# Performance work log

Measured on AMD Instinct MI355X. Metric: run time of the kernel, lower is better.

The kernel has to match this reference:

```python
import jax, jax.numpy as jnp
import numpy as np

N_NODES = 40000
N_EDGES = 640000
IN_CH, HID_CH, OUT_CH = 128, 128, 64


def setup_inputs() -> dict:
    key = jax.random.key(0)
    ks = jax.random.split(key, 8)
    x = jax.random.normal(ks[0], (N_NODES, IN_CH), dtype=jnp.float32)
    edge_index = jax.random.randint(ks[1], (2, N_EDGES), 0, N_NODES, dtype=jnp.int32)
    s = 1.0 / np.sqrt(IN_CH)
    W1_rel = jax.random.normal(ks[2], (HID_CH, IN_CH), dtype=jnp.float32) * s
    W1_root = jax.random.normal(ks[3], (HID_CH, IN_CH), dtype=jnp.float32) * s
    b1 = jnp.zeros((HID_CH,), dtype=jnp.float32)
    s2 = 1.0 / np.sqrt(HID_CH)
    W2_rel = jax.random.normal(ks[4], (OUT_CH, HID_CH), dtype=jnp.float32) * s2
    W2_root = jax.random.normal(ks[5], (OUT_CH, HID_CH), dtype=jnp.float32) * s2
    b2 = jnp.zeros((OUT_CH,), dtype=jnp.float32)
    return {"x": x, "edge_index": edge_index, "W1_rel": W1_rel, "W1_root": W1_root,
            "b1": b1, "W2_rel": W2_rel, "W2_root": W2_root, "b2": b2}


def graph_conv(x, edge_index, W_rel, W_root, b):
    # PyG GraphConv (aggr='add'): out_i = W_rel @ (sum_{j->i} x_j) + W_root @ x_i + b
    src, dst = edge_index[0], edge_index[1]
    agg = jax.ops.segment_sum(x[src], dst, num_segments=x.shape[0])  # [N, d_in]
    return agg @ W_rel.T + x @ W_root.T + b


def reference(x, edge_index, W1_rel, W1_root, b1, W2_rel, W2_root, b2):
    h = jax.nn.relu(graph_conv(x, edge_index, W1_rel, W1_root, b1))
    return graph_conv(h, edge_index, W2_rel, W2_root, b2)
```

## Files before the change

### kernel.cpp

```cpp
#include <hip/hip_runtime.h>

#define N_NODES 40000
#define N_EDGES 640000

typedef __attribute__((ext_vector_type(8))) short short8;
typedef __attribute__((ext_vector_type(4))) float f32x4;

__device__ __forceinline__ float b2f_hi(uint v) {
  uint u = v & 0xffff0000u;
  return __builtin_bit_cast(float, u);
}
__device__ __forceinline__ float b2f_lo(uint v) {
  uint u = v << 16;
  return __builtin_bit_cast(float, u);
}
__device__ __forceinline__ ushort f2b(float f) {
  uint u = __builtin_bit_cast(uint, f);
  u += 0x7fffu + ((u >> 16) & 1u);
  return (ushort)(u >> 16);
}

__global__ __launch_bounds__(256) void k_prep(
    const float* __restrict__ W1rel, const float* __restrict__ W1root,
    const float* __restrict__ W2rel, const float* __restrict__ W2root,
    ushort* __restrict__ Wb1, ushort* __restrict__ Wb2,
    int* __restrict__ deg) {
  const int b = blockIdx.x;
  if (b < 48) {
    const int i = (b * 256 + threadIdx.x) * 4;
    const float* src;
    ushort* dst;
    if (i < 32768) {
      dst = Wb1 + i;
      src = (i < 16384) ? (W1rel + i) : (W1root + (i - 16384));
    } else {
      int j = i - 32768;
      dst = Wb2 + j;
      src = (j < 8192) ? (W2rel + j) : (W2root + (j - 8192));
    }
    float4 v = *reinterpret_cast<const float4*>(src);
    uint2 o;
    o.x = (uint)f2b(v.x) | ((uint)f2b(v.y) << 16);
    o.y = (uint)f2b(v.z) | ((uint)f2b(v.w) << 16);
    *reinterpret_cast<uint2*>(dst) = o;
  } else {
    const int i = (b - 48) * 256 + threadIdx.x;
    if (i < N_NODES) deg[i] = 0;
  }
}

__global__ __launch_bounds__(256) void k_count(
    const int* __restrict__ ei, int* __restrict__ deg) {
  int e = blockIdx.x * 256 + threadIdx.x;
  atomicAdd(&deg[ei[N_EDGES + e]], 1);
}

__global__ __launch_bounds__(256) void k_scanA(
    const int* __restrict__ deg, int* __restrict__ local,
    int* __restrict__ bsum) {
  const int t = threadIdx.x;
  const int base = blockIdx.x * 1024 + t * 4;
  int v0 = 0, v1 = 0, v2 = 0, v3 = 0;
  if (base < N_NODES) {
    int4 v = *reinterpret_cast<const int4*>(deg + base);
    v0 = v.x; v1 = v.y; v2 = v.z; v3 = v.w;
  }
  const int tot = v0 + v1 + v2 + v3;
  const int lane = t & 63;
  int ws = tot;
#pragma unroll
  for (int off = 1; off < 64; off <<= 1) {
    int y = __shfl_up(ws, off, 64);
    if (lane >= off) ws += y;
  }
  __shared__ int wsum[4];
  if (lane == 63) wsum[t >> 6] = ws;
  __syncthreads();
  const int w = t >> 6;
  int wbase = 0;
#pragma unroll
  for (int i = 0; i < 4; ++i) wbase += (i < w) ? wsum[i] : 0;
  const int incl = wbase + ws;
  const int excl = incl - tot;
  if (base < N_NODES) {
    int4 o;
    o.x = excl;
    o.y = excl + v0;
    o.z = excl + v0 + v1;
    o.w = excl + v0 + v1 + v2;
    *reinterpret_cast<int4*>(local + base) = o;
  }
  if (t == 255) bsum[blockIdx.x] = incl;
}

__global__ __launch_bounds__(64) void k_scanB(
    const int* __restrict__ bsum, int* __restrict__ bbase) {
  const int t = threadIdx.x;
  int v = (t < 40) ? bsum[t] : 0;
  int ws = v;
#pragma unroll
  for (int off = 1; off < 64; off <<= 1) {
    int y = __shfl_up(ws, off, 64);
    if (t >= off) ws += y;
  }
  if (t < 40) bbase[t] = ws - v;
}

__global__ __launch_bounds__(256) void k_scanC(
    const int* __restrict__ local, const int* __restrict__ bbase,
    int* __restrict__ offs, int* __restrict__ cursor) {
  int i = blockIdx.x * 256 + threadIdx.x;
  if (i < N_NODES) {
    int v = local[i] + bbase[i >> 10];
    offs[i] = v;
    cursor[i] = v;
  }
  if (i == 0) offs[N_NODES] = N_EDGES;
}

__global__ __launch_bounds__(256) void k_fill(
    const int* __restrict__ ei, int* __restrict__ cursor,
    int* __restrict__ csr_src) {
  int e = blockIdx.x * 256 + threadIdx.x;
  int dst = ei[N_EDGES + e];
  int idx = atomicAdd(&cursor[dst], 1);
  csr_src[idx] = ei[e];
}

__global__ __launch_bounds__(256) void k_gemm1_mfma(
    const float* __restrict__ x, const ushort* __restrict__ Wb1,
    const float* __restrict__ b1, ushort* __restrict__ xr,
    ushort* __restrict__ xo) {
  const int t = threadIdx.x;
  const int lane = t & 63;
  const int n0 = blockIdx.x * 64 + (t >> 6) * 16;
  const int lr = lane & 15;
  const int hk = (lane >> 4) * 8;

  const float* arow = x + (size_t)(n0 + lr) * 128 + hk;
  short8 a[4];
#pragma unroll
  for (int c = 0; c < 4; ++c) {
    float4 f0 = *reinterpret_cast<const float4*>(arow + c * 32);
    float4 f1 = *reinterpret_cast<const float4*>(arow + c * 32 + 4);
    short8 v;
    v[0] = (short)f2b(f0.x); v[1] = (short)f2b(f0.y);
    v[2] = (short)f2b(f0.z); v[3] = (short)f2b(f0.w);
    v[4] = (short)f2b(f1.x); v[5] = (short)f2b(f1.y);
    v[6] = (short)f2b(f1.z); v[7] = (short)f2b(f1.w);
    a[c] = v;
  }

  const int orow = n0 + (lane >> 4) * 4;

#pragma unroll
  for (int ct = 0; ct < 16; ++ct) {
    const ushort* wrow = Wb1 + (size_t)(ct * 16 + lr) * 128 + hk;
    f32x4 acc = {0.f, 0.f, 0.f, 0.f};
    acc = __builtin_amdgcn_mfma_f32_16x16x32_bf16(
        a[0], *reinterpret_cast<const short8*>(wrow), acc, 0, 0, 0);
    acc = __builtin_amdgcn_mfma_f32_16x16x32_bf16(
        a[1], *reinterpret_cast<const short8*>(wrow + 32), acc, 0, 0, 0);
    acc = __builtin_amdgcn_mfma_f32_16x16x32_bf16(
        a[2], *reinterpret_cast<const short8*>(wrow + 64), acc, 0, 0, 0);
    acc = __builtin_amdgcn_mfma_f32_16x16x32_bf16(
        a[3], *reinterpret_cast<const short8*>(wrow + 96), acc, 0, 0, 0);

    if (ct < 8) {
      const int col = ct * 16 + lr;
#pragma unroll
      for (int i = 0; i < 4; ++i)
        xr[(size_t)(orow + i) * 128 + col] = f2b(acc[i]);
    } else {
      const int col = (ct - 8) * 16 + lr;
      const float bb = b1[col];
#pragma unroll
      for (int i = 0; i < 4; ++i)
        xo[(size_t)(orow + i) * 128 + col] = f2b(acc[i] + bb);
    }
  }
}

__global__ __launch_bounds__(256) void k_gather_relu(
    const ushort* __restrict__ xr, ushort* __restrict__ h,
    const int* __restrict__ csr_src, const int* __restrict__ offs) {
  int n = blockIdx.x * 4 + (threadIdx.x >> 6);
  n = __builtin_amdgcn_readfirstlane(n);
  const int lane = threadIdx.x & 63;
  const int s = offs[n], e = offs[n + 1];
  float s00 = 0.f, s01 = 0.f, s10 = 0.f, s11 = 0.f;
  float s20 = 0.f, s21 = 0.f, s30 = 0.f, s31 = 0.f;
  int i = s;
  for (; i + 3 < e; i += 4) {
    int e0 = csr_src[i], e1 = csr_src[i + 1];
    int e2 = csr_src[i + 2], e3 = csr_src[i + 3];
    uint v0 = *reinterpret_cast<const uint*>(xr + (size_t)e0 * 128 + lane * 2);
    uint v1 = *reinterpret_cast<const uint*>(xr + (size_t)e1 * 128 + lane * 2);
    uint v2 = *reinterpret_cast<const uint*>(xr + (size_t)e2 * 128 + lane * 2);
    uint v3 = *reinterpret_cast<const uint*>(xr + (size_t)e3 * 128 + lane * 2);
    s00 += b2f_lo(v0); s01 += b2f_hi(v0);
    s10 += b2f_lo(v1); s11 += b2f_hi(v1);
    s20 += b2f_lo(v2); s21 += b2f_hi(v2);
    s30 += b2f_lo(v3); s31 += b2f_hi(v3);
  }
  for (; i < e; ++i) {
    uint v = *reinterpret_cast<const uint*>(
        xr + (size_t)csr_src[i] * 128 + lane * 2);
    s00 += b2f_lo(v); s01 += b2f_hi(v);
  }
  const float g0 = (s00 + s10) + (s20 + s30);
  const float g1 = (s01 + s11) + (s21 + s31);
  ushort* hp = h + (size_t)n * 128 + lane * 2;
  uint xov = *reinterpret_cast<const uint*>(hp);
  float r0 = fmaxf(b2f_lo(xov) + g0, 0.f);
  float r1 = fmaxf(b2f_hi(xov) + g1, 0.f);
  *reinterpret_cast<uint*>(hp) = (uint)f2b(r0) | ((uint)f2b(r1) << 16);
}

__global__ __launch_bounds__(256) void k_gemm2_mfma(
    const ushort* __restrict__ h, const ushort* __restrict__ Wb2,
    const float* __restrict__ b2, ushort* __restrict__ t2,
    float* __restrict__ out) {
  const int t = threadIdx.x;
  const int lane = t & 63;
  const int n0 = blockIdx.x * 64 + (t >> 6) * 16;
  const int lr = lane & 15;
  const int hk = (lane >> 4) * 8;

  const ushort* arow = h + (size_t)(n0 + lr) * 128 + hk;
  const short8 a0 = *reinterpret_cast<const short8*>(arow);
  const short8 a1 = *reinterpret_cast<const short8*>(arow + 32);
  const short8 a2 = *reinterpret_cast<const short8*>(arow + 64);
  const short8 a3 = *reinterpret_cast<const short8*>(arow + 96);

  const int orow = n0 + (lane >> 4) * 4;

#pragma unroll
  for (int ct = 0; ct < 8; ++ct) {
    const ushort* wrow = Wb2 + (size_t)(ct * 16 + lr) * 128 + hk;
    f32x4 acc = {0.f, 0.f, 0.f, 0.f};
    acc = __builtin_amdgcn_mfma_f32_16x16x32_bf16(
        a0, *reinterpret_cast<const short8*>(wrow), acc, 0, 0, 0);
    acc = __builtin_amdgcn_mfma_f32_16x16x32_bf16(
        a1, *reinterpret_cast<const short8*>(wrow + 32), acc, 0, 0, 0);
    acc = __builtin_amdgcn_mfma_f32_16x16x32_bf16(
        a2, *reinterpret_cast<const short8*>(wrow + 64), acc, 0, 0, 0);
    acc = __builtin_amdgcn_mfma_f32_16x16x32_bf16(
        a3, *reinterpret_cast<const short8*>(wrow + 96), acc, 0, 0, 0);

    if (ct < 4) {
      const int col = ct * 16 + lr;
#pragma unroll
      for (int i = 0; i < 4; ++i)
        t2[(size_t)(orow + i) * 64 + col] = f2b(acc[i]);
    } else {
      const int col = (ct - 4) * 16 + lr;
      const float bb = b2[col];
#pragma unroll
      for (int i = 0; i < 4; ++i)
        out[(size_t)(orow + i) * 64 + col] = acc[i] + bb;
    }
  }
}

__global__ __launch_bounds__(256) void k_gather64(
    const ushort* __restrict__ t2, const int* __restrict__ csr_src,
    const int* __restrict__ offs, float* __restrict__ out) {
  int n = blockIdx.x * 4 + (threadIdx.x >> 6);
  n = __builtin_amdgcn_readfirstlane(n);
  const int lane = threadIdx.x & 63;
  const int s = offs[n], e = offs[n + 1];
  float a0 = 0.f, a1 = 0.f, a2 = 0.f, a3 = 0.f;
  int i = s;
  for (; i + 3 < e; i += 4) {
    int e0 = csr_src[i], e1 = csr_src[i + 1];
    int e2 = csr_src[i + 2], e3 = csr_src[i + 3];
    a0 += b2f_lo((uint)t2[(size_t)e0 * 64 + lane]);
    a1 += b2f_lo((uint)t2[(size_t)e1 * 64 + lane]);
    a2 += b2f_lo((uint)t2[(size_t)e2 * 64 + lane]);
    a3 += b2f_lo((uint)t2[(size_t)e3 * 64 + lane]);
  }
  for (; i < e; ++i)
    a0 += b2f_lo((uint)t2[(size_t)csr_src[i] * 64 + lane]);
  out[(size_t)n * 64 + lane] += (a0 + a1) + (a2 + a3);
}

extern "C" void kernel_launch(void* const* d_in, const int* in_sizes, int n_in,
                              void* d_out, int out_size, void* d_ws, size_t ws_size,
                              hipStream_t stream) {
  const float* x = (const float*)d_in[0];
  const int* ei = (const int*)d_in[1];
  const float* W1rel = (const float*)d_in[2];
  const float* W1root = (const float*)d_in[3];
  const float* b1 = (const float*)d_in[4];
  const float* W2rel = (const float*)d_in[5];
  const float* W2root = (const float*)d_in[6];
  const float* b2 = (const float*)d_in[7];
  float* out = (float*)d_out;

  ushort* xr = (ushort*)d_ws;
  ushort* xo = xr + (size_t)N_NODES * 128;
  ushort* t2 = xo + (size_t)N_NODES * 128;
  ushort* Wb1 = t2 + (size_t)N_NODES * 64;
  ushort* Wb2 = Wb1 + 32768;
  int* deg = (int*)(Wb2 + 16384);
  int* offs = deg + N_NODES;
  int* cursor = offs + (N_NODES + 1);
  int* csr_src = cursor + N_NODES;
  int* bsum = csr_src + N_EDGES;
  int* bbase = bsum + 64;
  int* local = (int*)xr;

  k_prep<<<205, 256, 0, stream>>>(W1rel, W1root, W2rel, W2root, Wb1, Wb2, deg);

  k_count<<<N_EDGES / 256, 256, 0, stream>>>(ei, deg);
  k_scanA<<<(N_NODES + 1023) / 1024, 256, 0, stream>>>(deg, local, bsum);
  k_scanB<<<1, 64, 0, stream>>>(bsum, bbase);
  k_scanC<<<(N_NODES + 255) / 256, 256, 0, stream>>>(local, bbase, offs, cursor);
  k_fill<<<N_EDGES / 256, 256, 0, stream>>>(ei, cursor, csr_src);

  k_gemm1_mfma<<<N_NODES / 64, 256, 0, stream>>>(x, Wb1, b1, xr, xo);
  k_gather_relu<<<N_NODES / 4, 256, 0, stream>>>(xr, xo, csr_src, offs);

  k_gemm2_mfma<<<N_NODES / 64, 256, 0, stream>>>(xo, Wb2, b2, t2, out);

  k_gather64<<<N_NODES / 4, 256, 0, stream>>>(t2, csr_src, offs, out);
}
```

Measured before the change: 234.9 us.

## Fuse degree count with GEMM1, merge scan stages, vectorize CSR gathers

Degree counting and the first MFMA GEMM become one launch, with block ranges split between the two jobs. The scanB step moves into scanC, where each block redoes the small block-sum scan in shared memory. Because xr is now written before the scan, the scan scratch moves to its own workspace region so it no longer aliases xr. Both gather kernels now have each quarter-wave fetch a different neighbor with 16B or 8B vector loads, then reduce across the quarters with shuffles. This cuts launch count and raises bytes per load, but only 16 lanes write the final output and the kernel does shuffle-reduction work.

```diff
diff --git a/kernel.cpp b/kernel.cpp
--- a/kernel.cpp
+++ b/kernel.cpp
@@ -49,10 +49,65 @@
   }
 }
 
-__global__ __launch_bounds__(256) void k_count(
-    const int* __restrict__ ei, int* __restrict__ deg) {
-  int e = blockIdx.x * 256 + threadIdx.x;
-  atomicAdd(&deg[ei[N_EDGES + e]], 1);
+__global__ __launch_bounds__(256) void k_count_gemm1(
+    const int* __restrict__ ei, int* __restrict__ deg,
+    const float* __restrict__ x, const ushort* __restrict__ Wb1,
+    const float* __restrict__ b1, ushort* __restrict__ xr,
+    ushort* __restrict__ xo) {
+  const int b = blockIdx.x;
+  if (b < 2500) {
+    int e = b * 256 + threadIdx.x;
+    atomicAdd(&deg[ei[N_EDGES + e]], 1);
+    return;
+  }
+  const int t = threadIdx.x;
+  const int lane = t & 63;
+  const int n0 = (b - 2500) * 64 + (t >> 6) * 16;
+  const int lr = lane & 15;
+  const int hk = (lane >> 4) * 8;
+
+  const float* arow = x + (size_t)(n0 + lr) * 128 + hk;
+  short8 a[4];
+#pragma unroll
+  for (int c = 0; c < 4; ++c) {
+    float4 f0 = *reinterpret_cast<const float4*>(arow + c * 32);
+    float4 f1 = *reinterpret_cast<const float4*>(arow + c * 32 + 4);
+    short8 v;
+    v[0] = (short)f2b(f0.x); v[1] = (short)f2b(f0.y);
+    v[2] = (short)f2b(f0.z); v[3] = (short)f2b(f0.w);
+    v[4] = (short)f2b(f1.x); v[5] = (short)f2b(f1.y);
+    v[6] = (short)f2b(f1.z); v[7] = (short)f2b(f1.w);
+    a[c] = v;
+  }
+
+  const int orow = n0 + (lane >> 4) * 4;
+
+#pragma unroll
+  for (int ct = 0; ct < 16; ++ct) {
+    const ushort* wrow = Wb1 + (size_t)(ct * 16 + lr) * 128 + hk;
+    f32x4 acc = {0.f, 0.f, 0.f, 0.f};
+    acc = __builtin_amdgcn_mfma_f32_16x16x32_bf16(
+        a[0], *reinterpret_cast<const short8*>(wrow), acc, 0, 0, 0);
+    acc = __builtin_amdgcn_mfma_f32_16x16x32_bf16(
+        a[1], *reinterpret_cast<const short8*>(wrow + 32), acc, 0, 0, 0);
+    acc = __builtin_amdgcn_mfma_f32_16x16x32_bf16(
+        a[2], *reinterpret_cast<const short8*>(wrow + 64), acc, 0, 0, 0);
+    acc = __builtin_amdgcn_mfma_f32_16x16x32_bf16(
+        a[3], *reinterpret_cast<const short8*>(wrow + 96), acc, 0, 0, 0);
+
+    if (ct < 8) {
+      const int col = ct * 16 + lr;
+#pragma unroll
+      for (int i = 0; i < 4; ++i)
+        xr[(size_t)(orow + i) * 128 + col] = f2b(acc[i]);
+    } else {
+      const int col = (ct - 8) * 16 + lr;
+      const float bb = b1[col];
+#pragma unroll
+      for (int i = 0; i < 4; ++i)
+        xo[(size_t)(orow + i) * 128 + col] = f2b(acc[i] + bb);
+    }
+  }
 }
 
 __global__ __launch_bounds__(256) void k_scanA(
@@ -93,25 +148,25 @@
   if (t == 255) bsum[blockIdx.x] = incl;
 }
 
-__global__ __launch_bounds__(64) void k_scanB(
-    const int* __restrict__ bsum, int* __restrict__ bbase) {
+__global__ __launch_bounds__(256) void k_scanC(
+    const int* __restrict__ local, const int* __restrict__ bsum,
+    int* __restrict__ offs, int* __restrict__ cursor) {
+  __shared__ int sb[40];
   const int t = threadIdx.x;
-  int v = (t < 40) ? bsum[t] : 0;
-  int ws = v;
-#pragma unroll
-  for (int off = 1; off < 64; off <<= 1) {
-    int y = __shfl_up(ws, off, 64);
-    if (t >= off) ws += y;
-  }
-  if (t < 40) bbase[t] = ws - v;
-}
-
-__global__ __launch_bounds__(256) void k_scanC(
-    const int* __restrict__ local, const int* __restrict__ bbase,
-    int* __restrict__ offs, int* __restrict__ cursor) {
-  int i = blockIdx.x * 256 + threadIdx.x;
+  if (t < 64) {
+    int v = (t < 40) ? bsum[t] : 0;
+    int ws = v;
+#pragma unroll
+    for (int off = 1; off < 64; off <<= 1) {
+      int y = __shfl_up(ws, off, 64);
+      if (t >= off) ws += y;
+    }
+    if (t < 40) sb[t] = ws - v;
+  }
+  __syncthreads();
+  int i = blockIdx.x * 256 + t;
   if (i < N_NODES) {
-    int v = local[i] + bbase[i >> 10];
+    int v = local[i] + sb[i >> 10];
     offs[i] = v;
     cursor[i] = v;
   }
@@ -127,94 +182,73 @@
   csr_src[idx] = ei[e];
 }
 
-__global__ __launch_bounds__(256) void k_gemm1_mfma(
-    const float* __restrict__ x, const ushort* __restrict__ Wb1,
-    const float* __restrict__ b1, ushort* __restrict__ xr,
-    ushort* __restrict__ xo) {
-  const int t = threadIdx.x;
-  const int lane = t & 63;
-  const int n0 = blockIdx.x * 64 + (t >> 6) * 16;
-  const int lr = lane & 15;
-  const int hk = (lane >> 4) * 8;
-
-  const float* arow = x + (size_t)(n0 + lr) * 128 + hk;
-  short8 a[4];
-#pragma unroll
-  for (int c = 0; c < 4; ++c) {
-    float4 f0 = *reinterpret_cast<const float4*>(arow + c * 32);
-    float4 f1 = *reinterpret_cast<const float4*>(arow + c * 32 + 4);
-    short8 v;
-    v[0] = (short)f2b(f0.x); v[1] = (short)f2b(f0.y);
-    v[2] = (short)f2b(f0.z); v[3] = (short)f2b(f0.w);
-    v[4] = (short)f2b(f1.x); v[5] = (short)f2b(f1.y);
-    v[6] = (short)f2b(f1.z); v[7] = (short)f2b(f1.w);
-    a[c] = v;
-  }
-
-  const int orow = n0 + (lane >> 4) * 4;
-
-#pragma unroll
-  for (int ct = 0; ct < 16; ++ct) {
-    const ushort* wrow = Wb1 + (size_t)(ct * 16 + lr) * 128 + hk;
-    f32x4 acc = {0.f, 0.f, 0.f, 0.f};
-    acc = __builtin_amdgcn_mfma_f32_16x16x32_bf16(
-        a[0], *reinterpret_cast<const short8*>(wrow), acc, 0, 0, 0);
-    acc = __builtin_amdgcn_mfma_f32_16x16x32_bf16(
-        a[1], *reinterpret_cast<const short8*>(wrow + 32), acc, 0, 0, 0);
-    acc = __builtin_amdgcn_mfma_f32_16x16x32_bf16(
-        a[2], *reinterpret_cast<const short8*>(wrow + 64), acc, 0, 0, 0);
-    acc = __builtin_amdgcn_mfma_f32_16x16x32_bf16(
-        a[3], *reinterpret_cast<const short8*>(wrow + 96), acc, 0, 0, 0);
-
-    if (ct < 8) {
-      const int col = ct * 16 + lr;
-#pragma unroll
-      for (int i = 0; i < 4; ++i)
-        xr[(size_t)(orow + i) * 128 + col] = f2b(acc[i]);
-    } else {
-      const int col = (ct - 8) * 16 + lr;
-      const float bb = b1[col];
-#pragma unroll
-      for (int i = 0; i < 4; ++i)
-        xo[(size_t)(orow + i) * 128 + col] = f2b(acc[i] + bb);
-    }
-  }
-}
-
 __global__ __launch_bounds__(256) void k_gather_relu(
     const ushort* __restrict__ xr, ushort* __restrict__ h,
     const int* __restrict__ csr_src, const int* __restrict__ offs) {
   int n = blockIdx.x * 4 + (threadIdx.x >> 6);
   n = __builtin_amdgcn_readfirstlane(n);
   const int lane = threadIdx.x & 63;
+  const int q = lane >> 4;
+  const int c8 = (lane & 15) << 3;
   const int s = offs[n], e = offs[n + 1];
-  float s00 = 0.f, s01 = 0.f, s10 = 0.f, s11 = 0.f;
-  float s20 = 0.f, s21 = 0.f, s30 = 0.f, s31 = 0.f;
+  float a[8] = {0.f, 0.f, 0.f, 0.f, 0.f, 0.f, 0.f, 0.f};
+  float b[8] = {0.f, 0.f, 0.f, 0.f, 0.f, 0.f, 0.f, 0.f};
   int i = s;
-  for (; i + 3 < e; i += 4) {
-    int e0 = csr_src[i], e1 = csr_src[i + 1];
-    int e2 = csr_src[i + 2], e3 = csr_src[i + 3];
-    uint v0 = *reinterpret_cast<const uint*>(xr + (size_t)e0 * 128 + lane * 2);
-    uint v1 = *reinterpret_cast<const uint*>(xr + (size_t)e1 * 128 + lane * 2);
-    uint v2 = *reinterpret_cast<const uint*>(xr + (size_t)e2 * 128 + lane * 2);
-    uint v3 = *reinterpret_cast<const uint*>(xr + (size_t)e3 * 128 + lane * 2);
-    s00 += b2f_lo(v0); s01 += b2f_hi(v0);
-    s10 += b2f_lo(v1); s11 += b2f_hi(v1);
-    s20 += b2f_lo(v2); s21 += b2f_hi(v2);
-    s30 += b2f_lo(v3); s31 += b2f_hi(v3);
-  }
-  for (; i < e; ++i) {
-    uint v = *reinterpret_cast<const uint*>(
-        xr + (size_t)csr_src[i] * 128 + lane * 2);
-    s00 += b2f_lo(v); s01 += b2f_hi(v);
-  }
-  const float g0 = (s00 + s10) + (s20 + s30);
-  const float g1 = (s01 + s11) + (s21 + s31);
-  ushort* hp = h + (size_t)n * 128 + lane * 2;
-  uint xov = *reinterpret_cast<const uint*>(hp);
-  float r0 = fmaxf(b2f_lo(xov) + g0, 0.f);
-  float r1 = fmaxf(b2f_hi(xov) + g1, 0.f);
-  *reinterpret_cast<uint*>(hp) = (uint)f2b(r0) | ((uint)f2b(r1) << 16);
+  for (; i + 7 < e; i += 8) {
+    int ea = csr_src[i + q];
+    int eb = csr_src[i + 4 + q];
+    uint4 va = *reinterpret_cast<const uint4*>(xr + (size_t)ea * 128 + c8);
+    uint4 vb = *reinterpret_cast<const uint4*>(xr + (size_t)eb * 128 + c8);
+    a[0] += b2f_lo(va.x); a[1] += b2f_hi(va.x);
+    a[2] += b2f_lo(va.y); a[3] += b2f_hi(va.y);
+    a[4] += b2f_lo(va.z); a[5] += b2f_hi(va.z);
+    a[6] += b2f_lo(va.w); a[7] += b2f_hi(va.w);
+    b[0] += b2f_lo(vb.x); b[1] += b2f_hi(vb.x);
+    b[2] += b2f_lo(vb.y); b[3] += b2f_hi(vb.y);
+    b[4] += b2f_lo(vb.z); b[5] += b2f_hi(vb.z);
+    b[6] += b2f_lo(vb.w); b[7] += b2f_hi(vb.w);
+  }
+  if (i + 3 < e) {
+    int ea = csr_src[i + q];
+    uint4 va = *reinterpret_cast<const uint4*>(xr + (size_t)ea * 128 + c8);
+    a[0] += b2f_lo(va.x); a[1] += b2f_hi(va.x);
+    a[2] += b2f_lo(va.y); a[3] += b2f_hi(va.y);
+    a[4] += b2f_lo(va.z); a[5] += b2f_hi(va.z);
+    a[6] += b2f_lo(va.w); a[7] += b2f_hi(va.w);
+    i += 4;
+  }
+  if (i < e && i + q < e) {
+    int ea = csr_src[i + q];
+    uint4 va = *reinterpret_cast<const uint4*>(xr + (size_t)ea * 128 + c8);
+    a[0] += b2f_lo(va.x); a[1] += b2f_hi(va.x);
+    a[2] += b2f_lo(va.y); a[3] += b2f_hi(va.y);
+    a[4] += b2f_lo(va.z); a[5] += b2f_hi(va.z);
+    a[6] += b2f_lo(va.w); a[7] += b2f_hi(va.w);
+  }
+#pragma unroll
+  for (int j = 0; j < 8; ++j) {
+    a[j] += b[j];
+    a[j] += __shfl_xor(a[j], 16, 64);
+    a[j] += __shfl_xor(a[j], 32, 64);
+  }
+  if (lane < 16) {
+    ushort* hp = h + (size_t)n * 128 + c8;
+    uint4 xov = *reinterpret_cast<const uint4*>(hp);
+    float r0 = fmaxf(b2f_lo(xov.x) + a[0], 0.f);
+    float r1 = fmaxf(b2f_hi(xov.x) + a[1], 0.f);
+    float r2 = fmaxf(b2f_lo(xov.y) + a[2], 0.f);
+    float r3 = fmaxf(b2f_hi(xov.y) + a[3], 0.f);
+    float r4 = fmaxf(b2f_lo(xov.z) + a[4], 0.f);
+    float r5 = fmaxf(b2f_hi(xov.z) + a[5], 0.f);
+    float r6 = fmaxf(b2f_lo(xov.w) + a[6], 0.f);
+    float r7 = fmaxf(b2f_hi(xov.w) + a[7], 0.f);
+    uint4 o;
+    o.x = (uint)f2b(r0) | ((uint)f2b(r1) << 16);
+    o.y = (uint)f2b(r2) | ((uint)f2b(r3) << 16);
+    o.z = (uint)f2b(r4) | ((uint)f2b(r5) << 16);
+    o.w = (uint)f2b(r6) | ((uint)f2b(r7) << 16);
+    *reinterpret_cast<uint4*>(hp) = o;
+  }
 }
 
 __global__ __launch_bounds__(256) void k_gemm2_mfma(
@@ -269,20 +303,47 @@
   int n = blockIdx.x * 4 + (threadIdx.x >> 6);
   n = __builtin_amdgcn_readfirstlane(n);
   const int lane = threadIdx.x & 63;
+  const int q = lane >> 4;
+  const int c4 = (lane & 15) << 2;
   const int s = offs[n], e = offs[n + 1];
-  float a0 = 0.f, a1 = 0.f, a2 = 0.f, a3 = 0.f;
+  float a[4] = {0.f, 0.f, 0.f, 0.f};
+  float b[4] = {0.f, 0.f, 0.f, 0.f};
   int i = s;
-  for (; i + 3 < e; i += 4) {
-    int e0 = csr_src[i], e1 = csr_src[i + 1];
-    int e2 = csr_src[i + 2], e3 = csr_src[i + 3];
-    a0 += b2f_lo((uint)t2[(size_t)e0 * 64 + lane]);
-    a1 += b2f_lo((uint)t2[(size_t)e1 * 64 + lane]);
-    a2 += b2f_lo((uint)t2[(size_t)e2 * 64 + lane]);
-    a3 += b2f_lo((uint)t2[(size_t)e3 * 64 + lane]);
-  }
-  for (; i < e; ++i)
-    a0 += b2f_lo((uint)t2[(size_t)csr_src[i] * 64 + lane]);
-  out[(size_t)n * 64 + lane] += (a0 + a1) + (a2 + a3);
+  for (; i + 7 < e; i += 8) {
+    int ea = csr_src[i + q];
+    int eb = csr_src[i + 4 + q];
+    uint2 va = *reinterpret_cast<const uint2*>(t2 + (size_t)ea * 64 + c4);
+    uint2 vb = *reinterpret_cast<const uint2*>(t2 + (size_t)eb * 64 + c4);
+    a[0] += b2f_lo(va.x); a[1] += b2f_hi(va.x);
+    a[2] += b2f_lo(va.y); a[3] += b2f_hi(va.y);
+    b[0] += b2f_lo(vb.x); b[1] += b2f_hi(vb.x);
+    b[2] += b2f_lo(vb.y); b[3] += b2f_hi(vb.y);
+  }
+  if (i + 3 < e) {
+    int ea = csr_src[i + q];
+    uint2 va = *reinterpret_cast<const uint2*>(t2 + (size_t)ea * 64 + c4);
+    a[0] += b2f_lo(va.x); a[1] += b2f_hi(va.x);
+    a[2] += b2f_lo(va.y); a[3] += b2f_hi(va.y);
+    i += 4;
+  }
+  if (i < e && i + q < e) {
+    int ea = csr_src[i + q];
+    uint2 va = *reinterpret_cast<const uint2*>(t2 + (size_t)ea * 64 + c4);
+    a[0] += b2f_lo(va.x); a[1] += b2f_hi(va.x);
+    a[2] += b2f_lo(va.y); a[3] += b2f_hi(va.y);
+  }
+#pragma unroll
+  for (int j = 0; j < 4; ++j) {
+    a[j] += b[j];
+    a[j] += __shfl_xor(a[j], 16, 64);
+    a[j] += __shfl_xor(a[j], 32, 64);
+  }
+  if (lane < 16) {
+    float4* op = reinterpret_cast<float4*>(out + (size_t)n * 64 + c4);
+    float4 cur = *op;
+    cur.x += a[0]; cur.y += a[1]; cur.z += a[2]; cur.w += a[3];
+    *op = cur;
+  }
 }
 
 extern "C" void kernel_launch(void* const* d_in, const int* in_sizes, int n_in,
@@ -308,18 +369,16 @@
   int* cursor = offs + (N_NODES + 1);
   int* csr_src = cursor + N_NODES;
   int* bsum = csr_src + N_EDGES;
-  int* bbase = bsum + 64;
-  int* local = (int*)xr;
+  int* local = bsum + 64;
 
   k_prep<<<205, 256, 0, stream>>>(W1rel, W1root, W2rel, W2root, Wb1, Wb2, deg);
 
-  k_count<<<N_EDGES / 256, 256, 0, stream>>>(ei, deg);
+  k_count_gemm1<<<3125, 256, 0, stream>>>(ei, deg, x, Wb1, b1, xr, xo);
+
   k_scanA<<<(N_NODES + 1023) / 1024, 256, 0, stream>>>(deg, local, bsum);
-  k_scanB<<<1, 64, 0, stream>>>(bsum, bbase);
-  k_scanC<<<(N_NODES + 255) / 256, 256, 0, stream>>>(local, bbase, offs, cursor);
+  k_scanC<<<(N_NODES + 255) / 256, 256, 0, stream>>>(local, bsum, offs, cursor);
   k_fill<<<N_EDGES / 256, 256, 0, stream>>>(ei, cursor, csr_src);
 
-  k_gemm1_mfma<<<N_NODES / 64, 256, 0, stream>>>(x, Wb1, b1, xr, xo);
   k_gather_relu<<<N_NODES / 4, 256, 0, stream>>>(xr, xo, csr_src, offs);
 
   k_gemm2_mfma<<<N_NODES / 64, 256, 0, stream>>>(xo, Wb2, b2, t2, out);
```

Result: no change. 234.6 us (-0.2%).
